# Kernel tuning notes

Measured on AMD Instinct MI355X. Metric: run time of the kernel, lower is better.

Reference implementation:

```python
import jax, jax.numpy as jnp
import numpy as np

N = 50000   # num_of_nodes (cfg.dataset.num_nodes)
C = 128     # in_channels; TopKPooling ratio = C/N -> k = C pooled nodes
E = 800000  # num edges


def setup_inputs() -> dict:
    key = jax.random.key(0)
    ks = jax.random.split(key, 8)
    std = 1.0 / np.sqrt(C)
    X = jax.random.normal(ks[0], (N, C), dtype=jnp.float32)
    edge_index = jax.random.randint(ks[1], (2, E), 0, N, dtype=jnp.int64)
    edge_weight = jax.random.uniform(ks[2], (E,), dtype=jnp.float32)
    p = jax.random.normal(ks[3], (C,), dtype=jnp.float32)                      # TopKPooling projection
    W_ih = jax.random.normal(ks[4], (3 * C, C), dtype=jnp.float32) * std       # GRU input weights [r|z|n]
    W_hh = jax.random.normal(ks[5], (3 * C, C), dtype=jnp.float32) * std       # GRU hidden weights
    b_ih = jnp.zeros((3 * C,), dtype=jnp.float32)
    b_hh = jnp.zeros((3 * C,), dtype=jnp.float32)
    W_conv = jax.random.uniform(ks[6], (C, C), dtype=jnp.float32, minval=-std, maxval=std)  # GCN lin weight
    b_conv = jnp.zeros((C,), dtype=jnp.float32)
    return {"X": X, "edge_weight": edge_weight, "p": p, "W_ih": W_ih, "W_hh": W_hh,
            "b_ih": b_ih, "b_hh": b_hh, "W_conv": W_conv, "b_conv": b_conv,
            "edge_index": edge_index}


def _forward(X, edge_weight, p, W_ih, W_hh, b_ih, b_hh, W_conv, b_conv, edge_index):
    # ---- TopKPooling: score = X.p/||p||, pick top k=C nodes, gate with tanh ----
    score = X @ p / jnp.linalg.norm(p)                       # [N]
    top_vals, top_idx = jax.lax.top_k(score, C)              # k = C (ratio = C/N)
    X_tilde = X[top_idx] * jnp.tanh(top_vals)[:, None]       # [C, C]
    X_tilde = jax.lax.stop_gradient(X_tilde)                 # .detach() in original

    # ---- GRU single step: input X_tilde (batch=C), hidden h0 = W_conv ----
    gi = X_tilde @ W_ih.T + b_ih                             # [C, 3C]
    gh = W_conv @ W_hh.T + b_hh                              # [C, 3C]
    gi_r, gi_z, gi_n = jnp.split(gi, 3, axis=-1)
    gh_r, gh_z, gh_n = jnp.split(gh, 3, axis=-1)
    r = jax.nn.sigmoid(gi_r + gh_r)
    z = jax.nn.sigmoid(gi_z + gh_z)
    n = jnp.tanh(gi_n + r * gh_n)
    W_new = (1.0 - z) * n + z * W_conv                       # evolved GCN weight [C, C]

    # ---- GCNConv with self-loops + symmetric normalization ----
    src, dst = edge_index[0], edge_index[1]
    loop = jnp.arange(N, dtype=src.dtype)
    src2 = jnp.concatenate([src, loop])
    dst2 = jnp.concatenate([dst, loop])
    w2 = jnp.concatenate([edge_weight, jnp.ones((N,), dtype=edge_weight.dtype)])
    deg = jax.ops.segment_sum(w2, dst2, num_segments=N)      # [N]
    dinv = jnp.where(deg > 0, jax.lax.rsqrt(deg), 0.0)
    norm = dinv[src2] * w2 * dinv[dst2]                      # [E+N]
    Xw = X @ W_new.T                                         # [N, C]
    msg = Xw[src2] * norm[:, None]                           # gather + scale, [E+N, C]
    out = jax.ops.segment_sum(msg, dst2, num_segments=N)     # scatter-add, [N, C]
    return out + b_conv


def reference(X, edge_weight, p, W_ih, W_hh, b_ih, b_hh, W_conv, b_conv, edge_index):
    return _forward(X, edge_weight, p, W_ih, W_hh, b_ih, b_hh, W_conv, b_conv, edge_index)
```

## Files before the change

kernel.cpp:

```cpp
#include <hip/hip_runtime.h>
#include <hip/hip_fp16.h>
#include <math.h>

#define C 128
#define HB 2048
#define NS 4096
#define SHB 192

typedef __attribute__((ext_vector_type(8))) short bf16x8;
typedef __attribute__((ext_vector_type(4))) float f32x4;

__device__ inline unsigned ord_f32(float f) {
    unsigned u = __float_as_uint(f);
    return u ^ ((u & 0x80000000u) ? 0xFFFFFFFFu : 0x80000000u);
}
__device__ inline float unord_f32(unsigned u) {
    return __uint_as_float(u ^ ((u & 0x80000000u) ? 0x80000000u : 0xFFFFFFFFu));
}
__device__ inline short f2bf(float f) {
    unsigned u = __float_as_uint(f);
    return (short)((u + 0x7FFFu + ((u >> 16) & 1u)) >> 16);
}
__device__ inline float bf2f(short s) {
    return __uint_as_float(((unsigned)(unsigned short)s) << 16);
}

__global__ __launch_bounds__(1024) void k_front(const float* __restrict__ X,
                                                const float* __restrict__ p,
                                                float* __restrict__ scores,
                                                int* __restrict__ hist,
                                                const int* __restrict__ ei,
                                                int* __restrict__ rh,
                                                int N, int E, int NBIN, int NBLKE) {
    int t = threadIdx.x;
    if (blockIdx.x < SHB) {
        __shared__ int lh[HB];
        for (int i = t; i < HB; i += 1024) lh[i] = 0;
        __syncthreads();
        int gw   = blockIdx.x * 16 + (t >> 6);
        int lane = t & 63;
        const float2* p2 = (const float2*)p;
        float2 pv2 = p2[lane];
        for (int r = gw; r < N; r += SHB * 16) {
            const float2* xr = (const float2*)(X + (size_t)r * C);
            float2 x2 = xr[lane];
            float a = x2.x * pv2.x + x2.y * pv2.y;
            #pragma unroll
            for (int o = 32; o; o >>= 1) a += __shfl_down(a, o);
            if (lane == 0) {
                scores[r] = a;
                atomicAdd(&lh[ord_f32(a) >> 21], 1);
            }
        }
        __syncthreads();
        for (int i = t; i < HB; i += 1024) {
            int v = lh[i];
            if (v) atomicAdd(&hist[i], v);
        }
    } else {
        __shared__ int bh[8][256];
        int cp = (t >> 7) & 7;
        for (int i = t; i < 8 * 256; i += 1024) ((int*)bh)[i] = 0;
        __syncthreads();
        int eb = blockIdx.x - SHB;
        int e = eb * 2048 + t * 2;
        if (e + 1 < E) {
            int2 d2 = *(const int2*)(ei + E + e);
            atomicAdd(&bh[cp][d2.x >> 8], 1);
            atomicAdd(&bh[cp][d2.y >> 8], 1);
        } else if (e < E) {
            atomicAdd(&bh[cp][ei[E + e] >> 8], 1);
        }
        __syncthreads();
        for (int i = t; i < NBIN; i += 1024) {
            int s = 0;
            #pragma unroll
            for (int c = 0; c < 8; c++) s += bh[c][i];
            rh[(size_t)i * NBLKE + eb] = s;
        }
    }
}

__global__ __launch_bounds__(512) void k_rscanA(int* __restrict__ rh, int* __restrict__ tot, int NBLKE) {
    __shared__ int sc[512];
    int t = threadIdx.x;
    int bin = blockIdx.x;
    int v = (t < NBLKE) ? rh[(size_t)bin * NBLKE + t] : 0;
    sc[t] = v;
    __syncthreads();
    for (int off = 1; off < 512; off <<= 1) {
        int u = (t >= off) ? sc[t - off] : 0;
        __syncthreads();
        sc[t] += u;
        __syncthreads();
    }
    if (t < NBLKE) rh[(size_t)bin * NBLKE + t] = sc[t] - v;
    if (t == 511) tot[bin] = sc[511];
}

__global__ __launch_bounds__(1024) void k_rscat(const int* __restrict__ ei, const float* __restrict__ ew,
                                                const int* __restrict__ rh, const int* __restrict__ tot,
                                                unsigned long long* __restrict__ sorted,
                                                int E, int NBIN, int NBLKE) {
    __shared__ int sc[256];
    __shared__ int cur[256];
    int t = threadIdx.x;
    int eb = blockIdx.x;
    int v = 0;
    if (t < 256) {
        v = (t < NBIN) ? tot[t] : 0;
        sc[t] = v;
    }
    __syncthreads();
    for (int off = 1; off < 256; off <<= 1) {
        int u = (t < 256 && t >= off) ? sc[t - off] : 0;
        __syncthreads();
        if (t < 256) sc[t] += u;
        __syncthreads();
    }
    if (t < NBIN) cur[t] = (sc[t] - v) + rh[(size_t)t * NBLKE + eb];
    __syncthreads();
    int e = eb * 2048 + t * 2;
    #pragma unroll
    for (int j = 0; j < 2; j++) {
        int ee = e + j;
        if (ee < E) {
            int s = ei[ee], d = ei[E + ee];
            float w = ew[ee];
            int pos = atomicAdd(&cur[d >> 8], 1);
            unsigned long long pk = ((unsigned long long)(unsigned)d << 48)
                                  | ((unsigned long long)(unsigned short)s << 32)
                                  |  (unsigned long long)__float_as_uint(w);
            sorted[pos] = pk;
        }
    }
}

__global__ __launch_bounds__(1024) void k_bin(const unsigned long long* __restrict__ sorted,
                                              const int* __restrict__ tot,
                                              int* __restrict__ offs, float* __restrict__ dinv,
                                              unsigned* __restrict__ epack,
                                              int N, int E, int NBIN) {
    __shared__ int cnt[256];
    __shared__ float wsum[256];
    __shared__ int sc[256];
    __shared__ int cur2[256];
    __shared__ int s_base[2];
    int t = threadIdx.x;
    int b = blockIdx.x;
    int v = 0;
    if (t < 256) {
        v = (t < NBIN) ? tot[t] : 0;
        sc[t] = v;
    }
    __syncthreads();
    for (int off = 1; off < 256; off <<= 1) {
        int u = (t < 256 && t >= off) ? sc[t - off] : 0;
        __syncthreads();
        if (t < 256) sc[t] += u;
        __syncthreads();
    }
    if (t == b) { s_base[0] = sc[t] - v; s_base[1] = sc[t]; }
    __syncthreads();
    int s0 = s_base[0], s1 = s_base[1];
    for (int i = t; i < 256; i += 1024) { cnt[i] = 0; wsum[i] = 0.f; }
    __syncthreads();
    for (int i = s0 + t; i < s1; i += 1024) {
        unsigned long long pk = sorted[i];
        int d8 = (int)(pk >> 48) & 255;
        float w = __uint_as_float((unsigned)(pk & 0xFFFFFFFFull));
        atomicAdd(&cnt[d8], 1);
        atomicAdd(&wsum[d8], w);
    }
    __syncthreads();
    int cv = (t < 256) ? cnt[t] : 0;
    if (t < 256) sc[t] = cv;
    __syncthreads();
    for (int off = 1; off < 256; off <<= 1) {
        int u = (t < 256 && t >= off) ? sc[t - off] : 0;
        __syncthreads();
        if (t < 256) sc[t] += u;
        __syncthreads();
    }
    if (t < 256) {
        int loff = sc[t] - cv;
        cur2[t] = s0 + loff;
        int node = b * 256 + t;
        if (node < N) {
            offs[node] = s0 + loff;
            dinv[node] = rsqrtf(1.0f + wsum[t]);
        }
    }
    if (b == NBIN - 1 && t == 0) offs[N] = E;
    __syncthreads();
    for (int i = s0 + t; i < s1; i += 1024) {
        unsigned long long pk = sorted[i];
        int d8 = (int)(pk >> 48) & 255;
        unsigned src = (unsigned)((pk >> 32) & 0xFFFFu);
        float w = __uint_as_float((unsigned)(pk & 0xFFFFFFFFull));
        int pos = atomicAdd(&cur2[d8], 1);
        __half hw = __float2half(w);
        epack[pos] = ((unsigned)*(unsigned short*)&hw << 16) | src;
    }
}

__global__ __launch_bounds__(256) void k_filter(const float* __restrict__ scores,
                                                const int* __restrict__ hist,
                                                int* __restrict__ nc,
                                                unsigned long long* __restrict__ cand, int N) {
    __shared__ int sc[256];
    __shared__ int sT;
    int t = threadIdx.x;
    int loc[8];
    int sum = 0;
    #pragma unroll
    for (int s = 0; s < 8; s++) {
        loc[s] = hist[HB - 1 - (t * 8 + s)];
        sum += loc[s];
    }
    sc[t] = sum;
    __syncthreads();
    for (int off = 1; off < 256; off <<= 1) {
        int v = (t >= off) ? sc[t - off] : 0;
        __syncthreads();
        sc[t] += v;
        __syncthreads();
    }
    int run = sc[t] - sum;
    #pragma unroll
    for (int s = 0; s < 8; s++) {
        int b = HB - 1 - (t * 8 + s);
        int nr = run + loc[s];
        if (run < C && nr >= C) sT = b;
        run = nr;
    }
    __syncthreads();
    int T = sT;
    int i = blockIdx.x * 256 + t;
    if (i < N) {
        unsigned u = ord_f32(scores[i]);
        if ((int)(u >> 21) >= T) {
            int pos = atomicAdd(nc, 1);
            if (pos < NS)
                cand[pos] = ((unsigned long long)u << 32) | (unsigned)(~(unsigned)i);
        }
    }
}

__global__ __launch_bounds__(1024) void k_sel(const unsigned long long* __restrict__ cand,
                                              const int* __restrict__ nc,
                                              const float* __restrict__ p,
                                              int* __restrict__ tidx, float* __restrict__ gate) {
    __shared__ unsigned long long sk[NS];
    __shared__ float red[16];
    __shared__ float s_pn;
    int t = threadIdx.x;
    int M = *nc; if (M > NS) M = NS;
    int S = 256; while (S < M) S <<= 1;
    for (int i = t; i < S; i += 1024) sk[i] = (i < M) ? cand[i] : 0ULL;
    float pv = 0.f;
    if (t < C) { float x = p[t]; pv = x * x; }
    #pragma unroll
    for (int o = 32; o; o >>= 1) pv += __shfl_down(pv, o);
    if ((t & 63) == 0) red[t >> 6] = pv;
    __syncthreads();
    if (t == 0) {
        float s = 0.f;
        for (int i = 0; i < 16; i++) s += red[i];
        s_pn = sqrtf(s);
    }
    for (int k = 2; k <= S; k <<= 1) {
        for (int j = k >> 1; j > 0; j >>= 1) {
            __syncthreads();
            for (int idx = t; idx < S; idx += 1024) {
                int l = idx ^ j;
                if (l > idx) {
                    unsigned long long a = sk[idx], b = sk[l];
                    bool desc = (idx & k) == 0;
                    if (desc ? (a < b) : (a > b)) { sk[idx] = b; sk[l] = a; }
                }
            }
        }
    }
    __syncthreads();
    if (t < C) {
        unsigned long long g = sk[t];
        tidx[t] = (int)(~(unsigned)(g & 0xFFFFFFFFull));
        gate[t] = tanhf(unord_f32((unsigned)(g >> 32)) / s_pn);
    }
}

__global__ __launch_bounds__(256) void k_gru(const float* __restrict__ X,
                                             const int* __restrict__ tidx,
                                             const float* __restrict__ gate,
                                             const float* __restrict__ Wc,
                                             const float* __restrict__ W_ih, const float* __restrict__ W_hh,
                                             const float* __restrict__ b_ih, const float* __restrict__ b_hh,
                                             float* __restrict__ wnewT) {
    int t = threadIdx.x;
    int i = t & 127;
    int j = blockIdx.x * 2 + (t >> 7);
    int src = tidx[i];
    float g = gate[i];
    const float4* xr   = (const float4*)(X + (size_t)src * C);
    const float4* hr   = (const float4*)(Wc + (size_t)i * C);
    const float4* wri  = (const float4*)(W_ih + (size_t)j * C);
    const float4* wzi  = (const float4*)(W_ih + (size_t)(C + j) * C);
    const float4* wni  = (const float4*)(W_ih + (size_t)(2 * C + j) * C);
    const float4* wrh  = (const float4*)(W_hh + (size_t)j * C);
    const float4* wzh  = (const float4*)(W_hh + (size_t)(C + j) * C);
    const float4* wnh  = (const float4*)(W_hh + (size_t)(2 * C + j) * C);
    float gir = 0, giz = 0, gin = 0, ghr = 0, ghz = 0, ghn = 0;
    #pragma unroll 8
    for (int k4 = 0; k4 < C / 4; k4++) {
        float4 x = xr[k4], h = hr[k4], a;
        a = wri[k4]; gir += x.x * a.x + x.y * a.y + x.z * a.z + x.w * a.w;
        a = wzi[k4]; giz += x.x * a.x + x.y * a.y + x.z * a.z + x.w * a.w;
        a = wni[k4]; gin += x.x * a.x + x.y * a.y + x.z * a.z + x.w * a.w;
        a = wrh[k4]; ghr += h.x * a.x + h.y * a.y + h.z * a.z + h.w * a.w;
        a = wzh[k4]; ghz += h.x * a.x + h.y * a.y + h.z * a.z + h.w * a.w;
        a = wnh[k4]; ghn += h.x * a.x + h.y * a.y + h.z * a.z + h.w * a.w;
    }
    gir = g * gir + b_ih[j];         ghr += b_hh[j];
    giz = g * giz + b_ih[C + j];     ghz += b_hh[C + j];
    gin = g * gin + b_ih[2 * C + j]; ghn += b_hh[2 * C + j];
    float r = 1.f / (1.f + expf(-(gir + ghr)));
    float z = 1.f / (1.f + expf(-(giz + ghz)));
    float n = tanhf(gin + r * ghn);
    float wn = (1.f - z) * n + z * Wc[(size_t)i * C + j];
    wnewT[(size_t)j * C + i] = wn;
}

__global__ __launch_bounds__(256) void k_xw(const float* __restrict__ X,
                                            const float* __restrict__ wnewT,
                                            const float* __restrict__ dinv,
                                            unsigned* __restrict__ xwh, int N) {
    __shared__ short Bh[C * C];
    __shared__ short Bl[C * C];
    int t = threadIdx.x;
    for (int idx = t; idx < C * C; idx += 256) {
        int k = idx >> 7, c = idx & 127;
        float wv = wnewT[idx];
        short hi = f2bf(wv);
        float lo = wv - bf2f(hi);
        int pos = c * C + (k ^ ((c & 15) << 3));
        Bh[pos] = hi;
        Bl[pos] = f2bf(lo);
    }
    __syncthreads();

    int wave = t >> 6, lane = t & 63;
    int ln = lane & 15, quad = lane >> 4;
    int r0 = blockIdx.x * 128 + wave * 32;

    f32x4 acc[2][8];
    #pragma unroll
    for (int mt = 0; mt < 2; mt++)
        #pragma unroll
        for (int ct = 0; ct < 8; ct++) { acc[mt][ct][0] = 0.f; acc[mt][ct][1] = 0.f; acc[mt][ct][2] = 0.f; acc[mt][ct][3] = 0.f; }

    int row0 = r0 + ln;       if (row0 >= N) row0 = N - 1;
    int row1 = r0 + 16 + ln;  if (row1 >= N) row1 = N - 1;
    const float* xr0 = X + (size_t)row0 * C + quad * 8;
    const float* xr1 = X + (size_t)row1 * C + quad * 8;

    for (int ks = 0; ks < 4; ks++) {
        float a0[8], a1[8];
        *(float4*)&a0[0] = *(const float4*)(xr0 + ks * 32);
        *(float4*)&a0[4] = *(const float4*)(xr0 + ks * 32 + 4);
        *(float4*)&a1[0] = *(const float4*)(xr1 + ks * 32);
        *(float4*)&a1[4] = *(const float4*)(xr1 + ks * 32 + 4);
        bf16x8 a0h, a0l, a1h, a1l;
        #pragma unroll
        for (int j = 0; j < 8; j++) {
            short h0 = f2bf(a0[j]); a0h[j] = h0; a0l[j] = f2bf(a0[j] - bf2f(h0));
            short h1 = f2bf(a1[j]); a1h[j] = h1; a1l[j] = f2bf(a1[j] - bf2f(h1));
        }
        int kb = ks * 32 + quad * 8;
        int koff = kb ^ (ln << 3);
        #pragma unroll
        for (int ct = 0; ct < 8; ct++) {
            int pos = (ct * 16 + ln) * C + koff;
            bf16x8 bh = *(bf16x8*)&Bh[pos];
            bf16x8 bl = *(bf16x8*)&Bl[pos];
            acc[0][ct] = __builtin_amdgcn_mfma_f32_16x16x32_bf16(a0h, bh, acc[0][ct], 0, 0, 0);
            acc[0][ct] = __builtin_amdgcn_mfma_f32_16x16x32_bf16(a0l, bh, acc[0][ct], 0, 0, 0);
            acc[0][ct] = __builtin_amdgcn_mfma_f32_16x16x32_bf16(a0h, bl, acc[0][ct], 0, 0, 0);
            acc[1][ct] = __builtin_amdgcn_mfma_f32_16x16x32_bf16(a1h, bh, acc[1][ct], 0, 0, 0);
            acc[1][ct] = __builtin_amdgcn_mfma_f32_16x16x32_bf16(a1l, bh, acc[1][ct], 0, 0, 0);
            acc[1][ct] = __builtin_amdgcn_mfma_f32_16x16x32_bf16(a1h, bl, acc[1][ct], 0, 0, 0);
        }
    }

    __half* H = (__half*)xwh;
    #pragma unroll
    for (int mt = 0; mt < 2; mt++) {
        int rbase = r0 + mt * 16 + quad * 4;
        #pragma unroll
        for (int reg = 0; reg < 4; reg++) {
            int r = rbase + reg;
            if (r < N) {
                float dvr = dinv[r];
                #pragma unroll
                for (int ct = 0; ct < 8; ct++) {
                    int col = ct * 16 + ln;
                    H[(size_t)r * C + col] = __float2half(acc[mt][ct][reg] * dvr);
                }
            }
        }
    }
}

__global__ __launch_bounds__(256) void k_gather(const unsigned* __restrict__ xwh,
                                                const int* __restrict__ offs,
                                                const unsigned* __restrict__ epack,
                                                const float* __restrict__ dinv,
                                                const float* __restrict__ b_conv,
                                                float* __restrict__ out, int N) {
    int t = threadIdx.x;
    int v = blockIdx.x * 4 + (t >> 6);
    int lane = t & 63;
    if (v >= N) return;
    int h = lane >> 5;
    int q = lane & 31;
    float dv = dinv[v];

    float ax = 0.f, ay = 0.f, az = 0.f, aw = 0.f;
    if (h == 0) {
        uint2 sv = *(const uint2*)(xwh + (size_t)v * 64 + q * 2);
        __half2 s0 = *(__half2*)&sv.x, s1 = *(__half2*)&sv.y;
        ax = __low2float(s0); ay = __high2float(s0);
        az = __low2float(s1); aw = __high2float(s1);
    }

    int e0 = offs[v], e1 = offs[v + 1];
    for (int base = e0; base < e1; base += 64) {
        int m = e1 - base; if (m > 64) m = 64;
        unsigned pkl = (lane < m) ? __builtin_nontemporal_load(&epack[base + lane]) : 0u;
        int pairs = (m + 1) >> 1;
        int jj = 0;
        for (; jj + 3 < pairs; jj += 4) {
            unsigned pa[4]; uint2 rx[4];
            #pragma unroll
            for (int u = 0; u < 4; u++) pa[u] = __shfl(pkl, 2 * (jj + u) + h);
            #pragma unroll
            for (int u = 0; u < 4; u++)
                rx[u] = *(const uint2*)(xwh + (size_t)(pa[u] & 0xFFFFu) * 64 + q * 2);
            #pragma unroll
            for (int u = 0; u < 4; u++) {
                unsigned short hs = (unsigned short)(pa[u] >> 16);
                float nm = __half2float(*(__half*)&hs);
                __half2 r0 = *(__half2*)&rx[u].x;
                __half2 r1 = *(__half2*)&rx[u].y;
                ax += nm * __low2float(r0);  ay += nm * __high2float(r0);
                az += nm * __low2float(r1);  aw += nm * __high2float(r1);
            }
        }
        for (; jj < pairs; jj++) {
            unsigned pa = __shfl(pkl, 2 * jj + h);
            uint2 rx = *(const uint2*)(xwh + (size_t)(pa & 0xFFFFu) * 64 + q * 2);
            unsigned short hs = (unsigned short)(pa >> 16);
            float nm = __half2float(*(__half*)&hs);
            __half2 r0 = *(__half2*)&rx.x;
            __half2 r1 = *(__half2*)&rx.y;
            ax += nm * __low2float(r0);  ay += nm * __high2float(r0);
            az += nm * __low2float(r1);  aw += nm * __high2float(r1);
        }
    }

    ax += __shfl_xor(ax, 32);
    ay += __shfl_xor(ay, 32);
    az += __shfl_xor(az, 32);
    aw += __shfl_xor(aw, 32);

    if (h == 0) {
        const float* bbp = b_conv + q * 4;
        f32x4 o;
        o[0] = ax * dv + bbp[0];
        o[1] = ay * dv + bbp[1];
        o[2] = az * dv + bbp[2];
        o[3] = aw * dv + bbp[3];
        __builtin_nontemporal_store(o, (f32x4*)(out + (size_t)v * C + q * 4));
    }
}

extern "C" void kernel_launch(void* const* d_in, const int* in_sizes, int n_in,
                              void* d_out, int out_size, void* d_ws, size_t ws_size,
                              hipStream_t stream) {
    const float* X      = (const float*)d_in[0];
    const float* ew     = (const float*)d_in[1];
    const float* p      = (const float*)d_in[2];
    const float* W_ih   = (const float*)d_in[3];
    const float* W_hh   = (const float*)d_in[4];
    const float* b_ih   = (const float*)d_in[5];
    const float* b_hh   = (const float*)d_in[6];
    const float* W_conv = (const float*)d_in[7];
    const float* b_conv = (const float*)d_in[8];
    const int*   ei     = (const int*)d_in[9];
    const int N = in_sizes[0] / C;
    const int E = in_sizes[1];
    float* out = (float*)d_out;
    const int NB    = (N + 255) / 256;
    const int NBIN  = (N + 255) / 256;
    const int NBLKE = (E + 2047) / 2048;

    char* w = (char*)d_ws;
    auto alloc = [&](size_t bytes) -> void* {
        void* r = (void*)w;
        w += (bytes + 255) & ~(size_t)255;
        return r;
    };
    int*   hist   = (int*)alloc(HB * 4);
    int*   nc     = (int*)alloc(256);
    size_t zbytes = (size_t)(w - (char*)d_ws);
    float* scores = (float*)alloc((size_t)N * 4);
    float* dinv   = (float*)alloc((size_t)N * 4);
    int*   offs   = (int*)alloc((size_t)(N + 1) * 4);
    int*   rh     = (int*)alloc((size_t)NBIN * NBLKE * 4);
    int*   tot    = (int*)alloc((size_t)NBIN * 4);
    unsigned long long* cand = (unsigned long long*)alloc((size_t)NS * 8);
    int*   tidx   = (int*)alloc(C * 4);
    float* gate   = (float*)alloc(C * 4);
    float* wnewT  = (float*)alloc((size_t)C * C * 4);
    unsigned long long* sorted = (unsigned long long*)alloc((size_t)E * 8);
    unsigned* epack = (unsigned*)alloc((size_t)E * 4);
    unsigned* xwh = (unsigned*)alloc((size_t)N * 64 * 4);

    hipMemsetAsync(d_ws, 0, zbytes, stream);
    k_front<<<SHB + NBLKE, 1024, 0, stream>>>(X, p, scores, hist, ei, rh, N, E, NBIN, NBLKE);
    k_filter<<<NB, 256, 0, stream>>>(scores, hist, nc, cand, N);
    k_sel<<<1, 1024, 0, stream>>>(cand, nc, p, tidx, gate);
    k_gru<<<C / 2, 256, 0, stream>>>(X, tidx, gate, W_conv, W_ih, W_hh, b_ih, b_hh, wnewT);
    k_rscanA<<<NBIN, 512, 0, stream>>>(rh, tot, NBLKE);
    k_rscat<<<NBLKE, 1024, 0, stream>>>(ei, ew, rh, tot, sorted, E, NBIN, NBLKE);
    k_bin<<<NBIN, 1024, 0, stream>>>(sorted, tot, offs, dinv, epack, N, E, NBIN);
    k_xw<<<(N + 127) / 128, 256, 0, stream>>>(X, wnewT, dinv, xwh, N);
    k_gather<<<(N + 3) / 4, 256, 0, stream>>>(xwh, offs, epack, dinv, b_conv, out, N);
}
```

Measured before the change: 218.4 us.

## Replace two-pass radix bucketing with global atomic degree count and direct CSR scatter

The old path built a CSR in several steps: per-block bucket histograms, a bucket scan, a scatter into a 64-bit sorted buffer, and a per-bucket binning pass. The new path counts per-node in-degree with global atomics inside k_front, runs a single-block prefix scan, and scatters edges straight into epack with global atomic cursors, accumulating weight sums at the same time. dinv is now computed on the fly from wsum in the consumer kernels. This removes two kernels and the 8-byte intermediate buffer. In exchange it relies on heavy global atomic contention, a serial single-block scan over 50k nodes, and a non-deterministic edge order within each node.

```diff
diff --git a/kernel.cpp b/kernel.cpp
--- a/kernel.cpp
+++ b/kernel.cpp
@@ -30,8 +30,8 @@
                                                 float* __restrict__ scores,
                                                 int* __restrict__ hist,
                                                 const int* __restrict__ ei,
-                                                int* __restrict__ rh,
-                                                int N, int E, int NBIN, int NBLKE) {
+                                                int* __restrict__ deg,
+                                                int N, int E) {
     int t = threadIdx.x;
     if (blockIdx.x < SHB) {
         __shared__ int lh[HB];
@@ -58,149 +58,74 @@
             if (v) atomicAdd(&hist[i], v);
         }
     } else {
-        __shared__ int bh[8][256];
-        int cp = (t >> 7) & 7;
-        for (int i = t; i < 8 * 256; i += 1024) ((int*)bh)[i] = 0;
-        __syncthreads();
         int eb = blockIdx.x - SHB;
         int e = eb * 2048 + t * 2;
         if (e + 1 < E) {
             int2 d2 = *(const int2*)(ei + E + e);
-            atomicAdd(&bh[cp][d2.x >> 8], 1);
-            atomicAdd(&bh[cp][d2.y >> 8], 1);
+            atomicAdd(&deg[d2.x], 1);
+            atomicAdd(&deg[d2.y], 1);
         } else if (e < E) {
-            atomicAdd(&bh[cp][ei[E + e] >> 8], 1);
-        }
-        __syncthreads();
-        for (int i = t; i < NBIN; i += 1024) {
-            int s = 0;
-            #pragma unroll
-            for (int c = 0; c < 8; c++) s += bh[c][i];
-            rh[(size_t)i * NBLKE + eb] = s;
-        }
-    }
-}
-
-__global__ __launch_bounds__(512) void k_rscanA(int* __restrict__ rh, int* __restrict__ tot, int NBLKE) {
-    __shared__ int sc[512];
-    int t = threadIdx.x;
-    int bin = blockIdx.x;
-    int v = (t < NBLKE) ? rh[(size_t)bin * NBLKE + t] : 0;
-    sc[t] = v;
-    __syncthreads();
-    for (int off = 1; off < 512; off <<= 1) {
-        int u = (t >= off) ? sc[t - off] : 0;
-        __syncthreads();
-        sc[t] += u;
-        __syncthreads();
-    }
-    if (t < NBLKE) rh[(size_t)bin * NBLKE + t] = sc[t] - v;
-    if (t == 511) tot[bin] = sc[511];
-}
-
-__global__ __launch_bounds__(1024) void k_rscat(const int* __restrict__ ei, const float* __restrict__ ew,
-                                                const int* __restrict__ rh, const int* __restrict__ tot,
-                                                unsigned long long* __restrict__ sorted,
-                                                int E, int NBIN, int NBLKE) {
-    __shared__ int sc[256];
-    __shared__ int cur[256];
-    int t = threadIdx.x;
-    int eb = blockIdx.x;
-    int v = 0;
-    if (t < 256) {
-        v = (t < NBIN) ? tot[t] : 0;
-        sc[t] = v;
-    }
-    __syncthreads();
-    for (int off = 1; off < 256; off <<= 1) {
-        int u = (t < 256 && t >= off) ? sc[t - off] : 0;
-        __syncthreads();
-        if (t < 256) sc[t] += u;
-        __syncthreads();
-    }
-    if (t < NBIN) cur[t] = (sc[t] - v) + rh[(size_t)t * NBLKE + eb];
-    __syncthreads();
-    int e = eb * 2048 + t * 2;
-    #pragma unroll
-    for (int j = 0; j < 2; j++) {
-        int ee = e + j;
-        if (ee < E) {
-            int s = ei[ee], d = ei[E + ee];
-            float w = ew[ee];
-            int pos = atomicAdd(&cur[d >> 8], 1);
-            unsigned long long pk = ((unsigned long long)(unsigned)d << 48)
-                                  | ((unsigned long long)(unsigned short)s << 32)
-                                  |  (unsigned long long)__float_as_uint(w);
-            sorted[pos] = pk;
-        }
-    }
-}
-
-__global__ __launch_bounds__(1024) void k_bin(const unsigned long long* __restrict__ sorted,
-                                              const int* __restrict__ tot,
-                                              int* __restrict__ offs, float* __restrict__ dinv,
-                                              unsigned* __restrict__ epack,
-                                              int N, int E, int NBIN) {
-    __shared__ int cnt[256];
-    __shared__ float wsum[256];
-    __shared__ int sc[256];
-    __shared__ int cur2[256];
-    __shared__ int s_base[2];
-    int t = threadIdx.x;
-    int b = blockIdx.x;
-    int v = 0;
-    if (t < 256) {
-        v = (t < NBIN) ? tot[t] : 0;
-        sc[t] = v;
-    }
-    __syncthreads();
-    for (int off = 1; off < 256; off <<= 1) {
-        int u = (t < 256 && t >= off) ? sc[t - off] : 0;
-        __syncthreads();
-        if (t < 256) sc[t] += u;
-        __syncthreads();
-    }
-    if (t == b) { s_base[0] = sc[t] - v; s_base[1] = sc[t]; }
-    __syncthreads();
-    int s0 = s_base[0], s1 = s_base[1];
-    for (int i = t; i < 256; i += 1024) { cnt[i] = 0; wsum[i] = 0.f; }
-    __syncthreads();
-    for (int i = s0 + t; i < s1; i += 1024) {
-        unsigned long long pk = sorted[i];
-        int d8 = (int)(pk >> 48) & 255;
-        float w = __uint_as_float((unsigned)(pk & 0xFFFFFFFFull));
-        atomicAdd(&cnt[d8], 1);
-        atomicAdd(&wsum[d8], w);
-    }
-    __syncthreads();
-    int cv = (t < 256) ? cnt[t] : 0;
-    if (t < 256) sc[t] = cv;
-    __syncthreads();
-    for (int off = 1; off < 256; off <<= 1) {
-        int u = (t < 256 && t >= off) ? sc[t - off] : 0;
-        __syncthreads();
-        if (t < 256) sc[t] += u;
-        __syncthreads();
-    }
-    if (t < 256) {
-        int loff = sc[t] - cv;
-        cur2[t] = s0 + loff;
-        int node = b * 256 + t;
-        if (node < N) {
-            offs[node] = s0 + loff;
-            dinv[node] = rsqrtf(1.0f + wsum[t]);
-        }
-    }
-    if (b == NBIN - 1 && t == 0) offs[N] = E;
-    __syncthreads();
-    for (int i = s0 + t; i < s1; i += 1024) {
-        unsigned long long pk = sorted[i];
-        int d8 = (int)(pk >> 48) & 255;
-        unsigned src = (unsigned)((pk >> 32) & 0xFFFFu);
-        float w = __uint_as_float((unsigned)(pk & 0xFFFFFFFFull));
-        int pos = atomicAdd(&cur2[d8], 1);
-        __half hw = __float2half(w);
-        epack[pos] = ((unsigned)*(unsigned short*)&hw << 16) | src;
+            atomicAdd(&deg[ei[E + e]], 1);
+        }
+    }
+}
+
+__global__ __launch_bounds__(1024) void k_scan(const int* __restrict__ deg,
+                                               int* __restrict__ offs, int* __restrict__ cur,
+                                               int N, int E) {
+    __shared__ int bs[1024];
+    int t = threadIdx.x;
+    int T = (N + 1023) >> 10;
+    int base = t * T;
+    int s = 0;
+    for (int i = 0; i < T; i++) {
+        int v = base + i;
+        if (v < N) s += deg[v];
+    }
+    bs[t] = s;
+    __syncthreads();
+    for (int off = 1; off < 1024; off <<= 1) {
+        int u = (t >= off) ? bs[t - off] : 0;
+        __syncthreads();
+        bs[t] += u;
+        __syncthreads();
+    }
+    int run = bs[t] - s;
+    for (int i = 0; i < T; i++) {
+        int v = base + i;
+        if (v < N) {
+            int d = deg[v];
+            offs[v] = run;
+            cur[v]  = run;
+            run += d;
+        }
+    }
+    if (t == 0) offs[N] = E;
+}
+
+__global__ __launch_bounds__(1024) void k_scat(const int* __restrict__ ei, const float* __restrict__ ew,
+                                               int* __restrict__ cur, float* __restrict__ wsum,
+                                               unsigned* __restrict__ epack, int E) {
+    int e = blockIdx.x * 2048 + threadIdx.x * 2;
+    if (e + 1 < E) {
+        int2 s2 = *(const int2*)(ei + e);
+        int2 d2 = *(const int2*)(ei + E + e);
+        float2 w2 = *(const float2*)(ew + e);
+        int p0 = atomicAdd(&cur[d2.x], 1);
+        atomicAdd(&wsum[d2.x], w2.x);
+        __half h0 = __float2half(w2.x);
+        epack[p0] = ((unsigned)*(unsigned short*)&h0 << 16) | (unsigned)s2.x;
+        int p1 = atomicAdd(&cur[d2.y], 1);
+        atomicAdd(&wsum[d2.y], w2.y);
+        __half h1 = __float2half(w2.y);
+        epack[p1] = ((unsigned)*(unsigned short*)&h1 << 16) | (unsigned)s2.y;
+    } else if (e < E) {
+        int s = ei[e], d = ei[E + e];
+        float w = ew[e];
+        int p0 = atomicAdd(&cur[d], 1);
+        atomicAdd(&wsum[d], w);
+        __half h0 = __float2half(w);
+        epack[p0] = ((unsigned)*(unsigned short*)&h0 << 16) | (unsigned)s;
     }
 }
 
@@ -333,7 +258,7 @@
 
 __global__ __launch_bounds__(256) void k_xw(const float* __restrict__ X,
                                             const float* __restrict__ wnewT,
-                                            const float* __restrict__ dinv,
+                                            const float* __restrict__ wsum,
                                             unsigned* __restrict__ xwh, int N) {
     __shared__ short Bh[C * C];
     __shared__ short Bl[C * C];
@@ -400,7 +325,7 @@
         for (int reg = 0; reg < 4; reg++) {
             int r = rbase + reg;
             if (r < N) {
-                float dvr = dinv[r];
+                float dvr = rsqrtf(1.0f + wsum[r]);
                 #pragma unroll
                 for (int ct = 0; ct < 8; ct++) {
                     int col = ct * 16 + ln;
@@ -414,7 +339,7 @@
 __global__ __launch_bounds__(256) void k_gather(const unsigned* __restrict__ xwh,
                                                 const int* __restrict__ offs,
                                                 const unsigned* __restrict__ epack,
-                                                const float* __restrict__ dinv,
+                                                const float* __restrict__ wsum,
                                                 const float* __restrict__ b_conv,
                                                 float* __restrict__ out, int N) {
     int t = threadIdx.x;
@@ -423,7 +348,7 @@
     if (v >= N) return;
     int h = lane >> 5;
     int q = lane & 31;
-    float dv = dinv[v];
+    float dv = rsqrtf(1.0f + wsum[v]);
 
     float ax = 0.f, ay = 0.f, az = 0.f, aw = 0.f;
     if (h == 0) {
@@ -501,7 +426,6 @@
     const int E = in_sizes[1];
     float* out = (float*)d_out;
     const int NB    = (N + 255) / 256;
-    const int NBIN  = (N + 255) / 256;
     const int NBLKE = (E + 2047) / 2048;
 
     char* w = (char*)d_ws;
@@ -512,28 +436,26 @@
     };
     int*   hist   = (int*)alloc(HB * 4);
     int*   nc     = (int*)alloc(256);
+    int*   deg    = (int*)alloc((size_t)N * 4);
+    float* wsum   = (float*)alloc((size_t)N * 4);
     size_t zbytes = (size_t)(w - (char*)d_ws);
     float* scores = (float*)alloc((size_t)N * 4);
-    float* dinv   = (float*)alloc((size_t)N * 4);
     int*   offs   = (int*)alloc((size_t)(N + 1) * 4);
-    int*   rh     = (int*)alloc((size_t)NBIN * NBLKE * 4);
-    int*   tot    = (int*)alloc((size_t)NBIN * 4);
+    int*   cur    = (int*)alloc((size_t)N * 4);
     unsigned long long* cand = (unsigned long long*)alloc((size_t)NS * 8);
     int*   tidx   = (int*)alloc(C * 4);
     float* gate   = (float*)alloc(C * 4);
     float* wnewT  = (float*)alloc((size_t)C * C * 4);
-    unsigned long long* sorted = (unsigned long long*)alloc((size_t)E * 8);
     unsigned* epack = (unsigned*)alloc((size_t)E * 4);
     unsigned* xwh = (unsigned*)alloc((size_t)N * 64 * 4);
 
     hipMemsetAsync(d_ws, 0, zbytes, stream);
-    k_front<<<SHB + NBLKE, 1024, 0, stream>>>(X, p, scores, hist, ei, rh, N, E, NBIN, NBLKE);
+    k_front<<<SHB + NBLKE, 1024, 0, stream>>>(X, p, scores, hist, ei, deg, N, E);
     k_filter<<<NB, 256, 0, stream>>>(scores, hist, nc, cand, N);
     k_sel<<<1, 1024, 0, stream>>>(cand, nc, p, tidx, gate);
     k_gru<<<C / 2, 256, 0, stream>>>(X, tidx, gate, W_conv, W_ih, W_hh, b_ih, b_hh, wnewT);
-    k_rscanA<<<NBIN, 512, 0, stream>>>(rh, tot, NBLKE);
-    k_rscat<<<NBLKE, 1024, 0, stream>>>(ei, ew, rh, tot, sorted, E, NBIN, NBLKE);
-    k_bin<<<NBIN, 1024, 0, stream>>>(sorted, tot, offs, dinv, epack, N, E, NBIN);
-    k_xw<<<(N + 127) / 128, 256, 0, stream>>>(X, wnewT, dinv, xwh, N);
-    k_gather<<<(N + 3) / 4, 256, 0, stream>>>(xwh, offs, epack, dinv, b_conv, out, N);
-}
+    k_scan<<<1, 1024, 0, stream>>>(deg, offs, cur, N, E);
+    k_scat<<<NBLKE, 1024, 0, stream>>>(ei, ew, cur, wsum, epack, E);
+    k_xw<<<(N + 127) / 128, 256, 0, stream>>>(X, wnewT, wsum, xwh, N);
+    k_gather<<<(N + 3) / 4, 256, 0, stream>>>(xwh, offs, epack, wsum, b_conv, out, N);
+}
```

Result: slower. 423.6 us (+93.9%).
